# Optimization experiments

Hardware: AMD Instinct MI355X
Metric: run time of the kernel (lower is better)

Reference implementation:

```python
import jax, jax.numpy as jnp
import numpy as np
import math

B, C, H, W = 16, 512, 32, 32
HEADS = 8
HD = C // HEADS            # 64 head_dim
NFREQ = HD // 4            # 16 (head_dim % 4 == 0)
MAX_FREQ = 128.0
T = H * W                  # 1024 tokens


def _make_so2_mat():
    # make_2dcoord: meshgrid('ij') of arange(H), arange(W) -> [H, W, 2]
    xg, yg = np.meshgrid(np.arange(H, dtype=np.float32), np.arange(W, dtype=np.float32), indexing='ij')
    coord = np.stack([xg, yg], -1)                                   # [H, W, 2]
    freqs = np.exp(np.linspace(0.0, math.log(MAX_FREQ), NFREQ)).astype(np.float32)  # [NFREQ]
    th = coord[..., None, :] * freqs[None, None, :, None]            # [H, W, NFREQ, 2]
    c, s = np.cos(th), np.sin(th)
    # rotation matrices [[c, -s], [s, c]] -> [H, W, NFREQ, 2(dim), 2, 2]
    mat = np.stack([np.stack([c, -s], -1), np.stack([s, c], -1)], -2)
    mat = mat.reshape(H * W, NFREQ * 2, 2, 2)                        # flatten(2,3) then flatten(0,1)
    return jnp.asarray(mat[:, : HD // 2])                            # [T, HD//2, 2, 2]


def setup_inputs() -> dict:
    key = jax.random.key(0)
    ks = jax.random.split(key, 5)
    mat = _make_so2_mat()
    return {
        'x': jax.random.normal(ks[0], (B, C, H, W), dtype=jnp.float32),
        'w_qkv': jax.random.normal(ks[1], (3 * C, C), dtype=jnp.float32) * 0.02,
        'b_qkv': jax.random.normal(ks[2], (3 * C,), dtype=jnp.float32) * 0.02,
        'w_o': jax.random.normal(ks[3], (C, C), dtype=jnp.float32) * 0.02,
        'b_o': jax.random.normal(ks[4], (C,), dtype=jnp.float32) * 0.02,
        'mat_q': mat,
        'mat_k': mat,
        'mat_v': mat,
        'mat_o': jnp.swapaxes(mat, -2, -1),
    }


def _rep_mul(rep, t):
    # rep: [T, HD//2, 2, 2]; t: [B, nh, T, HD] -> per-pair 2x2 rotation
    tb = t.reshape(B, HEADS, T, HD // 2, 2)
    return jnp.einsum('tfij,bntfj->bntfi', rep, tb).reshape(B, HEADS, T, HD)


def _split_heads(t):
    # 'b (c nh) h w -> b nh (h w) c' (c outer, nh inner in channel dim)
    return t.reshape(B, HD, HEADS, T).transpose(0, 2, 3, 1)


def reference(x, w_qkv, b_qkv, w_o, b_o, mat_q, mat_k, mat_v, mat_o):
    # 1x1 conv QKV projection == channel GEMM
    qkv = jnp.einsum('bchw,oc->bohw', x, w_qkv) + b_qkv[None, :, None, None]
    q, k, v = jnp.split(qkv, 3, axis=1)
    q, k, v = map(_split_heads, (q, k, v))                 # [B, nh, T, HD]
    q = _rep_mul(mat_q, q)
    k = _rep_mul(mat_k, k)
    v = _rep_mul(mat_v, v)
    scale = 1.0 / math.sqrt(HD)
    attn = jax.nn.softmax(jnp.einsum('bntd,bnsd->bnts', q, k) * scale, axis=-1)
    o = jnp.einsum('bnts,bnsd->bntd', attn, v)             # [B, nh, T, HD]
    o = _rep_mul(mat_o, o)
    # 'b nh (h w) c -> b (c nh) h w'
    o = o.reshape(B, HEADS, H, W, HD).transpose(0, 4, 1, 2, 3).reshape(B, C, H, W)
    return jnp.einsum('bchw,oc->bohw', o, w_o) + b_o[None, :, None, None]
```

## Files before the change

kernel.cpp:

```cpp
#include <hip/hip_runtime.h>


typedef __bf16 bf16x8 __attribute__((ext_vector_type(8)));
typedef __bf16 bf16x4 __attribute__((ext_vector_type(4)));
typedef float  f32x4  __attribute__((ext_vector_type(4)));

__device__ __forceinline__ f32x4 mfma16(bf16x8 a, bf16x8 b, f32x4 c) {
    return __builtin_amdgcn_mfma_f32_16x16x32_bf16(a, b, c, 0, 0, 0);
}

__device__ __forceinline__ void async16(const void* g, void* l) {
    __builtin_amdgcn_global_load_lds(
        (const __attribute__((address_space(1))) void*)g,
        (__attribute__((address_space(3))) void*)l, 16, 0, 0);
}

__global__ void k_convert_w(const float* __restrict__ wq, const float* __restrict__ wo,
                            __bf16* __restrict__ wqb, __bf16* __restrict__ wob) {
    int i = blockIdx.x * 256 + threadIdx.x;
    if (i < 3 * 512 * 512) wqb[i] = (__bf16)wq[i];
    if (i < 512 * 512) {
        int o = i >> 9, k2 = i & 511;
        int nh = k2 >> 6, hd = k2 & 63;
        wob[i] = (__bf16)wo[o * 512 + hd * 8 + nh];
    }
}

__global__ void k_transpose_x(const float* __restrict__ x, __bf16* __restrict__ xt) {
    __shared__ float tile[64][65];
    const int b  = blockIdx.z;
    const int c0 = blockIdx.y * 64;
    const int t0 = blockIdx.x * 64;
    const int tx = threadIdx.x, ty = threadIdx.y;
    const float* xp = x + ((size_t)b * 512 + c0) * 1024 + t0;
#pragma unroll
    for (int j = 0; j < 16; j++)
        tile[ty + j * 4][tx] = xp[(ty + j * 4) * 1024 + tx];
    __syncthreads();
    __bf16* xo = xt + ((size_t)b * 1024 + t0) * 512 + c0;
#pragma unroll
    for (int j = 0; j < 16; j++)
        xo[(ty + j * 4) * 512 + tx] = (__bf16)tile[tx][ty + j * 4];
}

__global__ __launch_bounds__(512) void k_gemm_qkv(
        const __bf16* __restrict__ A, const __bf16* __restrict__ W,
        const float* __restrict__ bias,
        const float* __restrict__ matq, const float* __restrict__ matk,
        const float* __restrict__ matv,
        __bf16* __restrict__ qd, __bf16* __restrict__ kd, __bf16* __restrict__ vtd)
{
    __shared__ __bf16 As[2][128][64];
    __shared__ __bf16 Bs[2][256][64];
    const int tid = threadIdx.x;
    const int id = blockIdx.x;
    const int logical = (id >> 3) + (id & 7) * 96;
    const int m0 = (logical / 6) * 128;
    const int jb = logical % 6;
    const int part = jb >> 1;
    const int nh_base = (jb & 1) * 4;
    const int lane = tid & 63, w = tid >> 6;
    const int ln = lane & 15, quad = lane >> 4;
    const int wr = w >> 2, wc = w & 3;

    const int srow = lane >> 3;
    const int scol = (((lane & 7) ^ srow) * 8);

    const __bf16* arow[2];
    const __bf16* brow[4];
#pragma unroll
    for (int jj = 0; jj < 2; jj++) {
        int rr = w * 16 + jj * 8 + srow;
        arow[jj] = &A[(size_t)(m0 + rr) * 512 + scol];
    }
#pragma unroll
    for (int jj = 0; jj < 4; jj++) {
        int rr = w * 32 + jj * 8 + srow;
        int o = part * 512 + (rr & 63) * 8 + nh_base + (rr >> 6);
        brow[jj] = &W[(size_t)o * 512 + scol];
    }

    f32x4 acc[4][4] = {};

#define STAGE_QKV(T, BUF)                                                   \
    do {                                                                    \
        const int _k0 = (T) * 64;                                           \
        _Pragma("unroll")                                                   \
        for (int jj = 0; jj < 2; jj++)                                      \
            async16(arow[jj] + _k0, &As[BUF][w * 16 + jj * 8][0]);          \
        _Pragma("unroll")                                                   \
        for (int jj = 0; jj < 4; jj++)                                      \
            async16(brow[jj] + _k0, &Bs[BUF][w * 32 + jj * 8][0]);          \
    } while (0)

    STAGE_QKV(0, 0);
    STAGE_QKV(1, 1);
    asm volatile("s_waitcnt vmcnt(6)" ::: "memory");
    __builtin_amdgcn_s_barrier();

#pragma unroll
    for (int t = 0; t < 8; ++t) {
        const int cur = t & 1;
        bf16x8 af[2][4], wf[2][4];
#pragma unroll
        for (int h = 0; h < 2; h++) {
#pragma unroll
            for (int mi = 0; mi < 4; mi++)
                af[h][mi] = *(const bf16x8*)&As[cur][wr * 64 + mi * 16 + ln][(((h * 4 + quad) ^ (ln & 7)) * 8)];
#pragma unroll
            for (int ni = 0; ni < 4; ni++)
                wf[h][ni] = *(const bf16x8*)&Bs[cur][wc * 64 + ni * 16 + ln][(((h * 4 + quad) ^ (ln & 7)) * 8)];
        }
        asm volatile("s_waitcnt lgkmcnt(0)" ::: "memory");
        __builtin_amdgcn_sched_barrier(0);
        __builtin_amdgcn_s_barrier();
        if (t < 6) STAGE_QKV(t + 2, cur);
        __builtin_amdgcn_s_setprio(1);
#pragma unroll
        for (int h = 0; h < 2; h++)
#pragma unroll
            for (int mi = 0; mi < 4; mi++)
#pragma unroll
                for (int ni = 0; ni < 4; ni++)
                    acc[mi][ni] = mfma16(af[h][mi], wf[h][ni], acc[mi][ni]);
        __builtin_amdgcn_s_setprio(0);
        if (t < 6) { asm volatile("s_waitcnt vmcnt(6)" ::: "memory"); }
        else       { asm volatile("s_waitcnt vmcnt(0)" ::: "memory"); }
        __builtin_amdgcn_s_barrier();
    }
#undef STAGE_QKV

    const int nh = nh_base + wc;
    const int rowbase = m0 + wr * 64;
    const int b  = rowbase >> 10, t0 = rowbase & 1023;
    const int bh = b * 8 + nh;
    const int ip = ln & 1;
    const float2* matp = (const float2*)(part == 0 ? matq : (part == 1 ? matk : matv));
    __bf16* qkdst = (part == 0) ? qd : kd;
    const float qscale = (part == 0) ? 0.18033688011112042f : 1.0f;

#pragma unroll
    for (int ni = 0; ni < 4; ni++) {
        const int hd = ni * 16 + ln;
        const int f  = hd >> 1;
        const float bias_o = bias[part * 512 + hd * 8 + nh];
#pragma unroll
        for (int mi = 0; mi < 4; mi++) {
            const int tq = t0 + mi * 16 + quad * 4;
            if (part < 2) {
#pragma unroll
                for (int r = 0; r < 4; r++) {
                    int t = tq + r;
                    float val = acc[mi][ni][r] + bias_o;
                    float pr  = __shfl_xor(val, 1);
                    float2 mv = matp[((size_t)t * 32 + f) * 2 + ip];
                    float e  = ip ? pr : val;
                    float oo = ip ? val : pr;
                    float rv = (mv.x * e + mv.y * oo) * qscale;
                    qkdst[((size_t)bh * 1024 + t) * 64 + hd] = (__bf16)rv;
                }
            } else {
                __bf16 pack[4];
#pragma unroll
                for (int r = 0; r < 4; r++) {
                    int t = tq + r;
                    float val = acc[mi][ni][r] + bias_o;
                    float pr  = __shfl_xor(val, 1);
                    float2 mv = matp[((size_t)t * 32 + f) * 2 + ip];
                    float e  = ip ? pr : val;
                    float oo = ip ? val : pr;
                    pack[r] = (__bf16)(mv.x * e + mv.y * oo);
                }
                *(uint2*)&vtd[((size_t)bh * 64 + hd) * 1024 + tq] = *(const uint2*)pack;
            }
        }
    }
}

__global__ __launch_bounds__(512) void k_attn(
        const __bf16* __restrict__ q, const __bf16* __restrict__ kk,
        const __bf16* __restrict__ vt, const float* __restrict__ mato,
        __bf16* __restrict__ od)
{
    __shared__ __bf16 Ks[64][64];
    __shared__ __bf16 Vs[64][64];
    __shared__ __bf16 Ps[8][32][64];
    const int id = blockIdx.x;
    const int logical = (id >> 3) + (id & 7) * 64;
    const int bh = logical >> 2, qt = logical & 3;
    const int tid = threadIdx.x, w = tid >> 6, lane = tid & 63;
    const int ln = lane & 15, quad = lane >> 4;
    const int lx = ln & 7;
    const int srow = lane >> 3;
    const int scol = ((lane & 7) ^ srow) * 8;
    const int qr0 = qt * 256 + w * 32;

    bf16x8 qa[2][2];
#pragma unroll
    for (int mi = 0; mi < 2; mi++)
#pragma unroll
        for (int ki = 0; ki < 2; ki++)
            qa[mi][ki] = *(const bf16x8*)&q[((size_t)bh * 1024 + qr0 + mi * 16 + ln) * 64 + ki * 32 + quad * 8];

    const __bf16* kbase = kk + (size_t)bh * 1024 * 64;
    const __bf16* vbase = vt + (size_t)bh * 64 * 1024;

    f32x4 oacc[2][4] = {};
    f32x4 lacc[2] = {};

    bf16x8 ones;
#pragma unroll
    for (int j = 0; j < 8; j++) ones[j] = (__bf16)1.0f;

    for (int st = 0; st < 16; st++) {
        async16(kbase + (size_t)(st * 64 + w * 8 + srow) * 64 + scol, &Ks[w * 8][0]);
        async16(vbase + (size_t)(w * 8 + srow) * 1024 + st * 64 + scol, &Vs[w * 8][0]);
        __syncthreads();

#pragma unroll
        for (int si = 0; si < 4; si++) {
            bf16x8 kb0 = *(const bf16x8*)&Ks[si * 16 + ln][((quad    ) ^ lx) * 8];
            bf16x8 kb1 = *(const bf16x8*)&Ks[si * 16 + ln][((quad + 4) ^ lx) * 8];
            f32x4 sc[2] = {};
#pragma unroll
            for (int mi = 0; mi < 2; mi++) {
                sc[mi] = mfma16(kb0, qa[mi][0], sc[mi]);
                sc[mi] = mfma16(kb1, qa[mi][1], sc[mi]);
            }
#pragma unroll
            for (int mi = 0; mi < 2; mi++) {
                bf16x4 pk;
#pragma unroll
                for (int r = 0; r < 4; r++)
                    pk[r] = (__bf16)exp2f(sc[mi][r]);
                *(bf16x4*)((char*)&Ps[w][mi * 16 + ln][0]
                           + (((si * 2 + (quad >> 1)) ^ lx) * 16) + (quad & 1) * 8) = pk;
            }
        }

#pragma unroll
        for (int kt = 0; kt < 2; kt++) {
            bf16x8 pa[2];
#pragma unroll
            for (int mi = 0; mi < 2; mi++)
                pa[mi] = *(const bf16x8*)&Ps[w][mi * 16 + ln][((kt * 4 + quad) ^ lx) * 8];
#pragma unroll
            for (int ni = 0; ni < 4; ni++) {
                bf16x8 vb = *(const bf16x8*)&Vs[ni * 16 + ln][((kt * 4 + quad) ^ lx) * 8];
                oacc[0][ni] = mfma16(vb, pa[0], oacc[0][ni]);
                oacc[1][ni] = mfma16(vb, pa[1], oacc[1][ni]);
            }
            lacc[0] = mfma16(ones, pa[0], lacc[0]);
            lacc[1] = mfma16(ones, pa[1], lacc[1]);
        }
        __syncthreads();
    }

    const float4* mo4 = (const float4*)mato;
#pragma unroll
    for (int mi = 0; mi < 2; mi++) {
        const int t = qr0 + mi * 16 + ln;
        const float invl = 1.0f / lacc[mi][0];
#pragma unroll
        for (int ni = 0; ni < 4; ni++) {
            const int hd0 = ni * 16 + quad * 4;
            const int f   = hd0 >> 1;
            float v0 = oacc[mi][ni][0] * invl;
            float v1 = oacc[mi][ni][1] * invl;
            float v2 = oacc[mi][ni][2] * invl;
            float v3 = oacc[mi][ni][3] * invl;
            float4 m1 = mo4[(size_t)t * 32 + f];
            float4 m2 = mo4[(size_t)t * 32 + f + 1];
            __bf16 pk[4];
            pk[0] = (__bf16)(m1.x * v0 + m1.y * v1);
            pk[1] = (__bf16)(m1.z * v0 + m1.w * v1);
            pk[2] = (__bf16)(m2.x * v2 + m2.y * v3);
            pk[3] = (__bf16)(m2.z * v2 + m2.w * v3);
            *(uint2*)&od[((size_t)bh * 1024 + t) * 64 + hd0] = *(const uint2*)pk;
        }
    }
}

__global__ __launch_bounds__(512) void k_gemm_out(
        const __bf16* __restrict__ A, const __bf16* __restrict__ W,
        const float* __restrict__ bias, float* __restrict__ out)
{
    __shared__ __bf16 As[2][128][64];
    __shared__ __bf16 Bs[2][256][64];
    const int tid = threadIdx.x;
    const int id = blockIdx.x;
    const int logical = (id >> 3) + (id & 7) * 32;
    const int m0 = (logical >> 1) * 128;
    const int n0 = (logical & 1) * 256;
    const int lane = tid & 63, w = tid >> 6;
    const int ln = lane & 15, quad = lane >> 4;
    const int wr = w >> 2, wc = w & 3;

    const int srow = lane >> 3;
    const int scol = (((lane & 7) ^ srow) * 8);

    const int bb = m0 >> 10, t00 = m0 & 1023;

    const __bf16* arow[2];
    const __bf16* brow[4];
#pragma unroll
    for (int jj = 0; jj < 2; jj++) {
        int rr = w * 16 + jj * 8 + srow;
        arow[jj] = &A[((size_t)bb * 8192 + t00 + rr) * 64 + scol];
    }
#pragma unroll
    for (int jj = 0; jj < 4; jj++) {
        int rr = w * 32 + jj * 8 + srow;
        brow[jj] = &W[(size_t)(n0 + rr) * 512 + scol];
    }

    f32x4 acc[4][4] = {};

#define STAGE_OUT(T, BUF)                                                   \
    do {                                                                    \
        const int _k0 = (T) * 64;                                           \
        _Pragma("unroll")                                                   \
        for (int jj = 0; jj < 2; jj++)                                      \
            async16(arow[jj] + (size_t)_k0 * 1024, &As[BUF][w * 16 + jj * 8][0]); \
        _Pragma("unroll")                                                   \
        for (int jj = 0; jj < 4; jj++)                                      \
            async16(brow[jj] + _k0, &Bs[BUF][w * 32 + jj * 8][0]);          \
    } while (0)

    STAGE_OUT(0, 0);
    STAGE_OUT(1, 1);
    asm volatile("s_waitcnt vmcnt(6)" ::: "memory");
    __builtin_amdgcn_s_barrier();

#pragma unroll
    for (int t = 0; t < 8; ++t) {
        const int cur = t & 1;
        bf16x8 af[2][4], wf[2][4];
#pragma unroll
        for (int h = 0; h < 2; h++) {
#pragma unroll
            for (int mi = 0; mi < 4; mi++)
                af[h][mi] = *(const bf16x8*)&As[cur][wr * 64 + mi * 16 + ln][(((h * 4 + quad) ^ (ln & 7)) * 8)];
#pragma unroll
            for (int ni = 0; ni < 4; ni++)
                wf[h][ni] = *(const bf16x8*)&Bs[cur][wc * 64 + ni * 16 + ln][(((h * 4 + quad) ^ (ln & 7)) * 8)];
        }
        asm volatile("s_waitcnt lgkmcnt(0)" ::: "memory");
        __builtin_amdgcn_sched_barrier(0);
        __builtin_amdgcn_s_barrier();
        if (t < 6) STAGE_OUT(t + 2, cur);
        __builtin_amdgcn_s_setprio(1);
#pragma unroll
        for (int h = 0; h < 2; h++)
#pragma unroll
            for (int mi = 0; mi < 4; mi++)
#pragma unroll
                for (int ni = 0; ni < 4; ni++)
                    acc[mi][ni] = mfma16(af[h][mi], wf[h][ni], acc[mi][ni]);
        __builtin_amdgcn_s_setprio(0);
        if (t < 6) { asm volatile("s_waitcnt vmcnt(6)" ::: "memory"); }
        else       { asm volatile("s_waitcnt vmcnt(0)" ::: "memory"); }
        __builtin_amdgcn_s_barrier();
    }
#undef STAGE_OUT

    const int rowbase = m0 + wr * 64;
    const int bb2 = rowbase >> 10, t0 = rowbase & 1023;
#pragma unroll
    for (int ni = 0; ni < 4; ni++) {
        int o = n0 + wc * 64 + ni * 16 + ln;
        float bias_o = bias[o];
#pragma unroll
        for (int mi = 0; mi < 4; mi++) {
            int t = t0 + mi * 16 + quad * 4;
            f32x4 v = acc[mi][ni];
            v[0] += bias_o; v[1] += bias_o; v[2] += bias_o; v[3] += bias_o;
            *(f32x4*)&out[((size_t)bb2 * 512 + o) * 1024 + t] = v;
        }
    }
}

extern "C" void kernel_launch(void* const* d_in, const int* in_sizes, int n_in,
                              void* d_out, int out_size, void* d_ws, size_t ws_size,
                              hipStream_t stream) {
    (void)in_sizes; (void)n_in; (void)out_size; (void)ws_size;
    const float* x     = (const float*)d_in[0];
    const float* w_qkv = (const float*)d_in[1];
    const float* b_qkv = (const float*)d_in[2];
    const float* w_o   = (const float*)d_in[3];
    const float* b_o   = (const float*)d_in[4];
    const float* mat_q = (const float*)d_in[5];
    const float* mat_k = (const float*)d_in[6];
    const float* mat_v = (const float*)d_in[7];
    const float* mat_o = (const float*)d_in[8];
    float* out = (float*)d_out;

    char* p = (char*)d_ws;
    __bf16* wqb = (__bf16*)p;  p += (size_t)3 * 512 * 512 * 2;
    __bf16* wob = (__bf16*)p;  p += (size_t)512 * 512 * 2;
    char* xt_base = p;
    __bf16* xt  = (__bf16*)p;  p += (size_t)16384 * 512 * 2;
    __bf16* qd  = (__bf16*)p;  p += (size_t)128 * 1024 * 64 * 2;
    __bf16* kd  = (__bf16*)p;  p += (size_t)128 * 1024 * 64 * 2;
    __bf16* vtd = (__bf16*)p;  p += (size_t)128 * 64 * 1024 * 2;
    __bf16* od  = (__bf16*)xt_base;

    k_convert_w  <<<dim3(3072),       dim3(256),    0, stream>>>(w_qkv, w_o, wqb, wob);
    k_transpose_x<<<dim3(16, 8, 16),  dim3(64, 4),  0, stream>>>(x, xt);
    k_gemm_qkv   <<<dim3(768),        dim3(512),    0, stream>>>(xt, wqb, b_qkv, mat_q, mat_k, mat_v, qd, kd, vtd);
    k_attn       <<<dim3(512),        dim3(512),    0, stream>>>(qd, kd, vtd, mat_o, od);
    k_gemm_out   <<<dim3(256),        dim3(512),    0, stream>>>(od, wob, b_o, out);
}
```

Baseline: 224.5 us.

## Enlarge QKV GEMM tile to 256 rows and keep attention probabilities in registers

The QKV projection GEMM now computes 256x256 tiles per block on a 2D grid of 384 blocks, where it used to compute 128x256 tiles on 768 blocks with swizzled block ids. This doubles per-block A staging and per-warp accumulators, so each weight tile is reused more. In the attention kernel, the exp'd score tile no longer goes through the LDS Ps buffer. It is repacked into MFMA A-operand layout in registers using permlane32/permlane16 swaps, which removes LDS writes and reads per tile. The trade-offs are higher register pressure, fewer blocks (a possible wave-quantization effect on 256 CUs), and no block-id swizzle for L2 locality.

```diff
diff --git a/kernel.cpp b/kernel.cpp
--- a/kernel.cpp
+++ b/kernel.cpp
@@ -4,6 +4,8 @@
 typedef __bf16 bf16x8 __attribute__((ext_vector_type(8)));
 typedef __bf16 bf16x4 __attribute__((ext_vector_type(4)));
 typedef float  f32x4  __attribute__((ext_vector_type(4)));
+typedef unsigned int uint2_t __attribute__((ext_vector_type(2)));
+typedef unsigned int uint4_t __attribute__((ext_vector_type(4)));
 
 __device__ __forceinline__ f32x4 mfma16(bf16x8 a, bf16x8 b, f32x4 c) {
     return __builtin_amdgcn_mfma_f32_16x16x32_bf16(a, b, c, 0, 0, 0);
@@ -13,6 +15,12 @@
     __builtin_amdgcn_global_load_lds(
         (const __attribute__((address_space(1))) void*)g,
         (__attribute__((address_space(3))) void*)l, 16, 0, 0);
+}
+
+__device__ __forceinline__ unsigned int pack2(float a, float b) {
+    unsigned short ua = __builtin_bit_cast(unsigned short, (__bf16)a);
+    unsigned short ub = __builtin_bit_cast(unsigned short, (__bf16)b);
+    return (unsigned int)ua | ((unsigned int)ub << 16);
 }
 
 __global__ void k_convert_w(const float* __restrict__ wq, const float* __restrict__ wo,
@@ -50,13 +58,11 @@
         const float* __restrict__ matv,
         __bf16* __restrict__ qd, __bf16* __restrict__ kd, __bf16* __restrict__ vtd)
 {
-    __shared__ __bf16 As[2][128][64];
+    __shared__ __bf16 As[2][256][64];
     __shared__ __bf16 Bs[2][256][64];
     const int tid = threadIdx.x;
-    const int id = blockIdx.x;
-    const int logical = (id >> 3) + (id & 7) * 96;
-    const int m0 = (logical / 6) * 128;
-    const int jb = logical % 6;
+    const int m0 = blockIdx.x * 256;
+    const int jb = blockIdx.y;
     const int part = jb >> 1;
     const int nh_base = (jb & 1) * 4;
     const int lane = tid & 63, w = tid >> 6;
@@ -66,28 +72,24 @@
     const int srow = lane >> 3;
     const int scol = (((lane & 7) ^ srow) * 8);
 
-    const __bf16* arow[2];
+    const __bf16* arow[4];
     const __bf16* brow[4];
-#pragma unroll
-    for (int jj = 0; jj < 2; jj++) {
-        int rr = w * 16 + jj * 8 + srow;
-        arow[jj] = &A[(size_t)(m0 + rr) * 512 + scol];
-    }
 #pragma unroll
     for (int jj = 0; jj < 4; jj++) {
         int rr = w * 32 + jj * 8 + srow;
+        arow[jj] = &A[(size_t)(m0 + rr) * 512 + scol];
         int o = part * 512 + (rr & 63) * 8 + nh_base + (rr >> 6);
         brow[jj] = &W[(size_t)o * 512 + scol];
     }
 
-    f32x4 acc[4][4] = {};
+    f32x4 acc[8][4] = {};
 
 #define STAGE_QKV(T, BUF)                                                   \
     do {                                                                    \
         const int _k0 = (T) * 64;                                           \
         _Pragma("unroll")                                                   \
-        for (int jj = 0; jj < 2; jj++)                                      \
-            async16(arow[jj] + _k0, &As[BUF][w * 16 + jj * 8][0]);          \
+        for (int jj = 0; jj < 4; jj++)                                      \
+            async16(arow[jj] + _k0, &As[BUF][w * 32 + jj * 8][0]);          \
         _Pragma("unroll")                                                   \
         for (int jj = 0; jj < 4; jj++)                                      \
             async16(brow[jj] + _k0, &Bs[BUF][w * 32 + jj * 8][0]);          \
@@ -95,18 +97,18 @@
 
     STAGE_QKV(0, 0);
     STAGE_QKV(1, 1);
-    asm volatile("s_waitcnt vmcnt(6)" ::: "memory");
+    asm volatile("s_waitcnt vmcnt(8)" ::: "memory");
     __builtin_amdgcn_s_barrier();
 
 #pragma unroll
     for (int t = 0; t < 8; ++t) {
         const int cur = t & 1;
-        bf16x8 af[2][4], wf[2][4];
+        bf16x8 af[2][8], wf[2][4];
 #pragma unroll
         for (int h = 0; h < 2; h++) {
 #pragma unroll
-            for (int mi = 0; mi < 4; mi++)
-                af[h][mi] = *(const bf16x8*)&As[cur][wr * 64 + mi * 16 + ln][(((h * 4 + quad) ^ (ln & 7)) * 8)];
+            for (int mi = 0; mi < 8; mi++)
+                af[h][mi] = *(const bf16x8*)&As[cur][wr * 128 + mi * 16 + ln][(((h * 4 + quad) ^ (ln & 7)) * 8)];
 #pragma unroll
             for (int ni = 0; ni < 4; ni++)
                 wf[h][ni] = *(const bf16x8*)&Bs[cur][wc * 64 + ni * 16 + ln][(((h * 4 + quad) ^ (ln & 7)) * 8)];
@@ -119,19 +121,19 @@
 #pragma unroll
         for (int h = 0; h < 2; h++)
 #pragma unroll
-            for (int mi = 0; mi < 4; mi++)
+            for (int mi = 0; mi < 8; mi++)
 #pragma unroll
                 for (int ni = 0; ni < 4; ni++)
                     acc[mi][ni] = mfma16(af[h][mi], wf[h][ni], acc[mi][ni]);
         __builtin_amdgcn_s_setprio(0);
-        if (t < 6) { asm volatile("s_waitcnt vmcnt(6)" ::: "memory"); }
+        if (t < 6) { asm volatile("s_waitcnt vmcnt(8)" ::: "memory"); }
         else       { asm volatile("s_waitcnt vmcnt(0)" ::: "memory"); }
         __builtin_amdgcn_s_barrier();
     }
 #undef STAGE_QKV
 
     const int nh = nh_base + wc;
-    const int rowbase = m0 + wr * 64;
+    const int rowbase = m0 + wr * 128;
     const int b  = rowbase >> 10, t0 = rowbase & 1023;
     const int bh = b * 8 + nh;
     const int ip = ln & 1;
@@ -145,7 +147,7 @@
         const int f  = hd >> 1;
         const float bias_o = bias[part * 512 + hd * 8 + nh];
 #pragma unroll
-        for (int mi = 0; mi < 4; mi++) {
+        for (int mi = 0; mi < 8; mi++) {
             const int tq = t0 + mi * 16 + quad * 4;
             if (part < 2) {
 #pragma unroll
@@ -184,7 +186,6 @@
 {
     __shared__ __bf16 Ks[64][64];
     __shared__ __bf16 Vs[64][64];
-    __shared__ __bf16 Ps[8][32][64];
     const int id = blockIdx.x;
     const int logical = (id >> 3) + (id & 7) * 64;
     const int bh = logical >> 2, qt = logical & 3;
@@ -217,24 +218,15 @@
         async16(vbase + (size_t)(w * 8 + srow) * 1024 + st * 64 + scol, &Vs[w * 8][0]);
         __syncthreads();
 
+        f32x4 sc[2][4] = {};
 #pragma unroll
         for (int si = 0; si < 4; si++) {
             bf16x8 kb0 = *(const bf16x8*)&Ks[si * 16 + ln][((quad    ) ^ lx) * 8];
             bf16x8 kb1 = *(const bf16x8*)&Ks[si * 16 + ln][((quad + 4) ^ lx) * 8];
-            f32x4 sc[2] = {};
 #pragma unroll
             for (int mi = 0; mi < 2; mi++) {
-                sc[mi] = mfma16(kb0, qa[mi][0], sc[mi]);
-                sc[mi] = mfma16(kb1, qa[mi][1], sc[mi]);
-            }
-#pragma unroll
-            for (int mi = 0; mi < 2; mi++) {
-                bf16x4 pk;
-#pragma unroll
-                for (int r = 0; r < 4; r++)
-                    pk[r] = (__bf16)exp2f(sc[mi][r]);
-                *(bf16x4*)((char*)&Ps[w][mi * 16 + ln][0]
-                           + (((si * 2 + (quad >> 1)) ^ lx) * 16) + (quad & 1) * 8) = pk;
+                sc[mi][si] = mfma16(kb0, qa[mi][0], sc[mi][si]);
+                sc[mi][si] = mfma16(kb1, qa[mi][1], sc[mi][si]);
             }
         }
 
@@ -242,8 +234,19 @@
         for (int kt = 0; kt < 2; kt++) {
             bf16x8 pa[2];
 #pragma unroll
-            for (int mi = 0; mi < 2; mi++)
-                pa[mi] = *(const bf16x8*)&Ps[w][mi * 16 + ln][((kt * 4 + quad) ^ lx) * 8];
+            for (int mi = 0; mi < 2; mi++) {
+                unsigned int u0 = pack2(exp2f(sc[mi][2 * kt][0]), exp2f(sc[mi][2 * kt][1]));
+                unsigned int u1 = pack2(exp2f(sc[mi][2 * kt][2]), exp2f(sc[mi][2 * kt][3]));
+                unsigned int v0 = pack2(exp2f(sc[mi][2 * kt + 1][0]), exp2f(sc[mi][2 * kt + 1][1]));
+                unsigned int v1 = pack2(exp2f(sc[mi][2 * kt + 1][2]), exp2f(sc[mi][2 * kt + 1][3]));
+                uint2_t r0 = __builtin_amdgcn_permlane32_swap(u0, v0, false, false);
+                uint2_t r1 = __builtin_amdgcn_permlane32_swap(u1, v1, false, false);
+                uint2_t s0 = __builtin_amdgcn_permlane16_swap(r0[0], r0[1], false, false);
+                uint2_t s1 = __builtin_amdgcn_permlane16_swap(r1[0], r1[1], false, false);
+                uint4_t pw;
+                pw[0] = s0[0]; pw[1] = s1[0]; pw[2] = s0[1]; pw[3] = s1[1];
+                pa[mi] = __builtin_bit_cast(bf16x8, pw);
+            }
 #pragma unroll
             for (int ni = 0; ni < 4; ni++) {
                 bf16x8 vb = *(const bf16x8*)&Vs[ni * 16 + ln][((kt * 4 + quad) ^ lx) * 8];
@@ -407,7 +410,7 @@
 
     k_convert_w  <<<dim3(3072),       dim3(256),    0, stream>>>(w_qkv, w_o, wqb, wob);
     k_transpose_x<<<dim3(16, 8, 16),  dim3(64, 4),  0, stream>>>(x, xt);
-    k_gemm_qkv   <<<dim3(768),        dim3(512),    0, stream>>>(xt, wqb, b_qkv, mat_q, mat_k, mat_v, qd, kd, vtd);
+    k_gemm_qkv   <<<dim3(64, 6),      dim3(512),    0, stream>>>(xt, wqb, b_qkv, mat_q, mat_k, mat_v, qd, kd, vtd);
     k_attn       <<<dim3(512),        dim3(512),    0, stream>>>(qd, kd, vtd, mat_o, od);
     k_gemm_out   <<<dim3(256),        dim3(512),    0, stream>>>(od, wob, b_o, out);
 }
```

New measurement: 237.1 us. +5.6%, slower.

## Merge prep kernels and interleave QKV GEMM loads with MFMA phases

Applied to the files above, without the earlier changes.

Fuses the weight conversion and input transpose into one launch, using the block index to pick the role, which removes one kernel launch. The QKV GEMM main loop is split into four MFMA phases, one per M sub-tile. The A-fragment LDS reads and the next-stage B and A global-to-LDS copies are issued between these phases, so memory traffic overlaps compute. This adds more barriers per iteration and depends on the hand-written waitcnt counts staying correct for the new issue order.

```diff
diff --git a/kernel.cpp b/kernel.cpp
--- a/kernel.cpp
+++ b/kernel.cpp
@@ -15,32 +15,34 @@
         (__attribute__((address_space(3))) void*)l, 16, 0, 0);
 }
 
-__global__ void k_convert_w(const float* __restrict__ wq, const float* __restrict__ wo,
-                            __bf16* __restrict__ wqb, __bf16* __restrict__ wob) {
-    int i = blockIdx.x * 256 + threadIdx.x;
-    if (i < 3 * 512 * 512) wqb[i] = (__bf16)wq[i];
-    if (i < 512 * 512) {
-        int o = i >> 9, k2 = i & 511;
-        int nh = k2 >> 6, hd = k2 & 63;
-        wob[i] = (__bf16)wo[o * 512 + hd * 8 + nh];
-    }
-}
-
-__global__ void k_transpose_x(const float* __restrict__ x, __bf16* __restrict__ xt) {
+__global__ void k_prep(const float* __restrict__ x, __bf16* __restrict__ xt,
+                       const float* __restrict__ wq, const float* __restrict__ wo,
+                       __bf16* __restrict__ wqb, __bf16* __restrict__ wob) {
     __shared__ float tile[64][65];
-    const int b  = blockIdx.z;
-    const int c0 = blockIdx.y * 64;
-    const int t0 = blockIdx.x * 64;
-    const int tx = threadIdx.x, ty = threadIdx.y;
-    const float* xp = x + ((size_t)b * 512 + c0) * 1024 + t0;
-#pragma unroll
-    for (int j = 0; j < 16; j++)
-        tile[ty + j * 4][tx] = xp[(ty + j * 4) * 1024 + tx];
-    __syncthreads();
-    __bf16* xo = xt + ((size_t)b * 1024 + t0) * 512 + c0;
-#pragma unroll
-    for (int j = 0; j < 16; j++)
-        xo[(ty + j * 4) * 512 + tx] = (__bf16)tile[tx][ty + j * 4];
+    const int id = blockIdx.x;
+    const int tid = threadIdx.x;
+    if (id < 2048) {
+        const int bx = id & 15, by = (id >> 4) & 7, bz = id >> 7;
+        const int c0 = by * 64, t0 = bx * 64;
+        const int tx = tid & 63, ty = tid >> 6;
+        const float* xp = x + ((size_t)bz * 512 + c0) * 1024 + t0;
+#pragma unroll
+        for (int j = 0; j < 16; j++)
+            tile[ty + j * 4][tx] = xp[(ty + j * 4) * 1024 + tx];
+        __syncthreads();
+        __bf16* xo = xt + ((size_t)bz * 1024 + t0) * 512 + c0;
+#pragma unroll
+        for (int j = 0; j < 16; j++)
+            xo[(ty + j * 4) * 512 + tx] = (__bf16)tile[tx][ty + j * 4];
+    } else {
+        int i = (id - 2048) * 256 + tid;
+        if (i < 3 * 512 * 512) wqb[i] = (__bf16)wq[i];
+        if (i < 512 * 512) {
+            int o = i >> 9, k2 = i & 511;
+            int nh = k2 >> 6, hd = k2 & 63;
+            wob[i] = (__bf16)wo[o * 512 + hd * 8 + nh];
+        }
+    }
 }
 
 __global__ __launch_bounds__(512) void k_gemm_qkv(
@@ -82,19 +84,23 @@
 
     f32x4 acc[4][4] = {};
 
-#define STAGE_QKV(T, BUF)                                                   \
+#define STAGE_A(T, BUF)                                                     \
     do {                                                                    \
         const int _k0 = (T) * 64;                                           \
         _Pragma("unroll")                                                   \
         for (int jj = 0; jj < 2; jj++)                                      \
             async16(arow[jj] + _k0, &As[BUF][w * 16 + jj * 8][0]);          \
+    } while (0)
+#define STAGE_B(T, BUF)                                                     \
+    do {                                                                    \
+        const int _k0 = (T) * 64;                                           \
         _Pragma("unroll")                                                   \
         for (int jj = 0; jj < 4; jj++)                                      \
             async16(brow[jj] + _k0, &Bs[BUF][w * 32 + jj * 8][0]);          \
     } while (0)
 
-    STAGE_QKV(0, 0);
-    STAGE_QKV(1, 1);
+    STAGE_A(0, 0); STAGE_B(0, 0);
+    STAGE_A(1, 1); STAGE_B(1, 1);
     asm volatile("s_waitcnt vmcnt(6)" ::: "memory");
     __builtin_amdgcn_s_barrier();
 
@@ -105,30 +111,60 @@
 #pragma unroll
         for (int h = 0; h < 2; h++) {
 #pragma unroll
-            for (int mi = 0; mi < 4; mi++)
+            for (int ni = 0; ni < 4; ni++)
+                wf[h][ni] = *(const bf16x8*)&Bs[cur][wc * 64 + ni * 16 + ln][(((h * 4 + quad) ^ (ln & 7)) * 8)];
+#pragma unroll
+            for (int mi = 0; mi < 2; mi++)
                 af[h][mi] = *(const bf16x8*)&As[cur][wr * 64 + mi * 16 + ln][(((h * 4 + quad) ^ (ln & 7)) * 8)];
-#pragma unroll
-            for (int ni = 0; ni < 4; ni++)
-                wf[h][ni] = *(const bf16x8*)&Bs[cur][wc * 64 + ni * 16 + ln][(((h * 4 + quad) ^ (ln & 7)) * 8)];
-        }
+        }
+        __builtin_amdgcn_s_barrier();
         asm volatile("s_waitcnt lgkmcnt(0)" ::: "memory");
         __builtin_amdgcn_sched_barrier(0);
-        __builtin_amdgcn_s_barrier();
-        if (t < 6) STAGE_QKV(t + 2, cur);
         __builtin_amdgcn_s_setprio(1);
 #pragma unroll
         for (int h = 0; h < 2; h++)
 #pragma unroll
-            for (int mi = 0; mi < 4; mi++)
-#pragma unroll
-                for (int ni = 0; ni < 4; ni++)
-                    acc[mi][ni] = mfma16(af[h][mi], wf[h][ni], acc[mi][ni]);
+            for (int ni = 0; ni < 4; ni++)
+                acc[0][ni] = mfma16(af[h][0], wf[h][ni], acc[0][ni]);
         __builtin_amdgcn_s_setprio(0);
-        if (t < 6) { asm volatile("s_waitcnt vmcnt(6)" ::: "memory"); }
-        else       { asm volatile("s_waitcnt vmcnt(0)" ::: "memory"); }
-        __builtin_amdgcn_s_barrier();
-    }
-#undef STAGE_QKV
+        __builtin_amdgcn_s_barrier();
+#pragma unroll
+        for (int h = 0; h < 2; h++)
+#pragma unroll
+            for (int mi = 2; mi < 4; mi++)
+                af[h][mi] = *(const bf16x8*)&As[cur][wr * 64 + mi * 16 + ln][(((h * 4 + quad) ^ (ln & 7)) * 8)];
+        if (t < 6) STAGE_B(t + 2, cur);
+        __builtin_amdgcn_s_barrier();
+        asm volatile("s_waitcnt lgkmcnt(0)" ::: "memory");
+        __builtin_amdgcn_sched_barrier(0);
+        __builtin_amdgcn_s_setprio(1);
+#pragma unroll
+        for (int h = 0; h < 2; h++)
+#pragma unroll
+            for (int ni = 0; ni < 4; ni++)
+                acc[1][ni] = mfma16(af[h][1], wf[h][ni], acc[1][ni]);
+        __builtin_amdgcn_s_setprio(0);
+        __builtin_amdgcn_s_barrier();
+        if (t < 6) STAGE_A(t + 2, cur);
+        __builtin_amdgcn_s_setprio(1);
+#pragma unroll
+        for (int h = 0; h < 2; h++)
+#pragma unroll
+            for (int ni = 0; ni < 4; ni++)
+                acc[2][ni] = mfma16(af[h][2], wf[h][ni], acc[2][ni]);
+        __builtin_amdgcn_s_setprio(0);
+        __builtin_amdgcn_s_setprio(1);
+#pragma unroll
+        for (int h = 0; h < 2; h++)
+#pragma unroll
+            for (int ni = 0; ni < 4; ni++)
+                acc[3][ni] = mfma16(af[h][3], wf[h][ni], acc[3][ni]);
+        __builtin_amdgcn_s_setprio(0);
+        if (t < 6)      { asm volatile("s_waitcnt vmcnt(6)" ::: "memory"); __builtin_amdgcn_s_barrier(); }
+        else if (t == 6){ asm volatile("s_waitcnt vmcnt(0)" ::: "memory"); __builtin_amdgcn_s_barrier(); }
+    }
+#undef STAGE_A
+#undef STAGE_B
 
     const int nh = nh_base + wc;
     const int rowbase = m0 + wr * 64;
@@ -405,9 +441,8 @@
     __bf16* vtd = (__bf16*)p;  p += (size_t)128 * 64 * 1024 * 2;
     __bf16* od  = (__bf16*)xt_base;
 
-    k_convert_w  <<<dim3(3072),       dim3(256),    0, stream>>>(w_qkv, w_o, wqb, wob);
-    k_transpose_x<<<dim3(16, 8, 16),  dim3(64, 4),  0, stream>>>(x, xt);
-    k_gemm_qkv   <<<dim3(768),        dim3(512),    0, stream>>>(xt, wqb, b_qkv, mat_q, mat_k, mat_v, qd, kd, vtd);
-    k_attn       <<<dim3(512),        dim3(512),    0, stream>>>(qd, kd, vtd, mat_o, od);
-    k_gemm_out   <<<dim3(256),        dim3(512),    0, stream>>>(od, wob, b_o, out);
-}
+    k_prep     <<<dim3(5120),    dim3(256), 0, stream>>>(x, xt, w_qkv, w_o, wqb, wob);
+    k_gemm_qkv <<<dim3(768),     dim3(512), 0, stream>>>(xt, wqb, b_qkv, mat_q, mat_k, mat_v, qd, kd, vtd);
+    k_attn     <<<dim3(512),     dim3(512), 0, stream>>>(qd, kd, vtd, mat_o, od);
+    k_gemm_out <<<dim3(256),     dim3(512), 0, stream>>>(od, wob, b_o, out);
+}
```

Measured after the change: 225.6 us. Within noise of the previous version (+0.5%).
